# Performance work log

Hardware: AMD Instinct MI355X
Metric: run time of the kernel (lower is better)

## Reference

```python
import jax, jax.numpy as jnp
import numpy as np

T, B, E, H = 128, 1024, 1024, 1024  # batch must equal hidden (original code uses Whh @ h)


def setup_inputs() -> dict:
    key = jax.random.key(0)
    ks = jax.random.split(key, 10)
    s = 1.0 / np.sqrt(H).astype(np.float32)  # ~xavier scale, avoids gate saturation
    inp = {
        'X': jax.random.normal(ks[0], (T, B, E), dtype=jnp.float32),
        'Wii': jax.random.normal(ks[1], (E, H), dtype=jnp.float32) * s,
        'Whi': jax.random.normal(ks[2], (H, H), dtype=jnp.float32) * s,
        'bi': jnp.zeros((H,), dtype=jnp.float32),
        'Wif': jax.random.normal(ks[3], (E, H), dtype=jnp.float32) * s,
        'Whf': jax.random.normal(ks[4], (H, H), dtype=jnp.float32) * s,
        'bf': jnp.zeros((H,), dtype=jnp.float32),
        'Wig': jax.random.normal(ks[5], (E, H), dtype=jnp.float32) * s,
        'Whg': jax.random.normal(ks[6], (H, H), dtype=jnp.float32) * s,
        'bg': jnp.zeros((H,), dtype=jnp.float32),
        'Wio': jax.random.normal(ks[7], (E, H), dtype=jnp.float32) * s,
        'Who': jax.random.normal(ks[8], (H, H), dtype=jnp.float32) * s,
        'bo': jnp.zeros((H,), dtype=jnp.float32),
    }
    return inp


def reference(X, Wii, Whi, bi, Wif, Whf, bf, Wig, Whg, bg, Wio, Who, bo):
    # Faithful to the original: recurrent term is Whh @ h (NOT h @ Whh),
    # which requires batch == hidden as in the source module.
    batch = X.shape[1]
    hid = Wii.shape[1]
    h0 = jnp.zeros((batch, hid), dtype=X.dtype)
    c0 = jnp.zeros((batch, hid), dtype=X.dtype)

    def step(carry, x_t):
        h, c = carry
        i = jax.nn.sigmoid(x_t @ Wii + Whi @ h + bi)
        f = jax.nn.sigmoid(x_t @ Wif + Whf @ h + bf)
        g = jnp.tanh(x_t @ Wig + Whg @ h + bg)
        o = jax.nn.sigmoid(x_t @ Wio + Who @ h + bo)
        c_new = f * c + i * g
        h_new = o * jnp.tanh(c_new)
        return (h_new, c_new), h_new

    (h_t, c_t), hidden_sequence = jax.lax.scan(step, (h0, c0), X)
    return hidden_sequence, (h_t, c_t)
```

## Files before the change

### kernel.cpp

```cpp
#include <hip/hip_runtime.h>
#include <cstdint>

typedef __attribute__((ext_vector_type(8))) short bf16x8;
typedef __attribute__((ext_vector_type(4))) float f32x4;
typedef __attribute__((ext_vector_type(4))) unsigned int u32x4;

#define AS1 __attribute__((address_space(1)))
#define AS3 __attribute__((address_space(3)))

__device__ __forceinline__ unsigned short f2bf(float f) {
  unsigned int u = __builtin_bit_cast(unsigned int, f);
  return (unsigned short)((u + 0x7fffu + ((u >> 16) & 1u)) >> 16);
}
__device__ __forceinline__ float bf2f(unsigned short h) {
  unsigned int u = ((unsigned int)h) << 16;
  return __builtin_bit_cast(float, u);
}
__device__ __forceinline__ float sigm(float x) { return 1.f / (1.f + __expf(-x)); }
__device__ __forceinline__ float tanh_f(float x) {
  float e = __expf(2.f * x);
  return 1.f - 2.f / (e + 1.f);
}
__device__ __forceinline__ void gload16(const void* g, void* l) {
  __builtin_amdgcn_global_load_lds((const AS1 unsigned int*)g, (AS3 unsigned int*)l, 16, 0, 0);
}
__device__ __forceinline__ int swz(int e) { return e ^ (((e >> 6) & 7) << 3); }


__global__ __launch_bounds__(256) void conv_wh_kernel(
    const float4* __restrict__ w0, const float4* __restrict__ w1,
    const float4* __restrict__ w2, const float4* __restrict__ w3,
    unsigned long long* __restrict__ dst) {
  int i = blockIdx.x * 256 + threadIdx.x;
  int g = i >> 18;
  const float4* s = g == 0 ? w0 : g == 1 ? w1 : g == 2 ? w2 : w3;
  float4 v = s[i & 0x3FFFF];
  unsigned long long p = (unsigned long long)f2bf(v.x) |
                         ((unsigned long long)f2bf(v.y) << 16) |
                         ((unsigned long long)f2bf(v.z) << 32) |
                         ((unsigned long long)f2bf(v.w) << 48);
  dst[i] = p;
}

__global__ __launch_bounds__(256) void conv_wiT_kernel(
    const float* __restrict__ w0, const float* __restrict__ w1,
    const float* __restrict__ w2, const float* __restrict__ w3,
    unsigned short* __restrict__ dst) {
  __shared__ unsigned short ls[64][72];
  int bid = blockIdx.x;
  int g = bid >> 8;
  int t2 = bid & 255;
  int tj = t2 & 15, tk = t2 >> 4;
  const float* W = g == 0 ? w0 : g == 1 ? w1 : g == 2 ? w2 : w3;
  int k0 = tk * 64, j0 = tj * 64;
  int ty = threadIdx.x >> 6, tx = threadIdx.x & 63;
#pragma unroll
  for (int r = 0; r < 16; ++r) {
    int k = k0 + ty * 16 + r;
    ls[tx][ty * 16 + r] = f2bf(W[k * 1024 + j0 + tx]);
  }
  __syncthreads();
#pragma unroll
  for (int r = 0; r < 16; ++r) {
    int jl = ty * 16 + r;
    dst[(size_t)(g * 1024 + j0 + jl) * 1024 + k0 + tx] = ls[jl][tx];
  }
}

__global__ __launch_bounds__(256) void conv_bias_kernel(
    const float* __restrict__ b0, const float* __restrict__ b1,
    const float* __restrict__ b2, const float* __restrict__ b3,
    float* __restrict__ dst) {
  int i = blockIdx.x * 256 + threadIdx.x;
  const float* s = (i >> 10) == 0 ? b0 : (i >> 10) == 1 ? b1 : (i >> 10) == 2 ? b2 : b3;
  dst[i] = s[i & 1023];
}

__global__ __launch_bounds__(256) void conv_x_kernel(
    const float4* __restrict__ src, unsigned long long* __restrict__ dst, int n4) {
  int i = blockIdx.x * 256 + threadIdx.x;
  if (i < n4) {
    float4 v = src[i];
    dst[i] = (unsigned long long)f2bf(v.x) |
             ((unsigned long long)f2bf(v.y) << 16) |
             ((unsigned long long)f2bf(v.z) << 32) |
             ((unsigned long long)f2bf(v.w) << 48);
  }
}

__global__ __launch_bounds__(512) void xproj_gemm_kernel(
    const unsigned short* __restrict__ A,
    const unsigned short* __restrict__ Bt,
    unsigned short* __restrict__ C,
    int Mc) {
  __shared__ __align__(16) unsigned short smem[2][2][256 * 64];
  int xcd = blockIdx.x & 7;
  int i5 = blockIdx.x >> 3;
  int bn = xcd * 2 + (i5 & 1);
  int bm = i5 >> 1;
  int m0 = bm * 256, n0 = bn * 256;
  int tid = threadIdx.x, w = tid >> 6, lane = tid & 63;
  int wm = w >> 2, wn = w & 3;
  int l15 = lane & 15, l4 = lane >> 4;

  f32x4 acc[8][4];
#pragma unroll
  for (int i = 0; i < 8; ++i)
#pragma unroll
    for (int j = 0; j < 4; ++j) acc[i][j] = (f32x4)0.f;

  auto stageHalf = [&](int buf, int kt, int X) {
    int kk = kt * 64;
    unsigned short* dst = &smem[buf][X & 1][0];
    const unsigned short* src = (X & 1) ? Bt : A;
    int gbase = (X & 1) ? n0 : m0;
    int r0 = (X >> 1) * 128;
#pragma unroll
    for (int u = 0; u < 2; ++u) {
      int cid = u * 512 + tid;
      int rl = r0 + (cid >> 3), s = cid & 7;
      int sk = kk + ((s ^ (rl & 7)) << 3);
      gload16(&src[(size_t)(gbase + rl) * 1024 + sk],
              &dst[r0 * 64 + (u * 512 + w * 64) * 8]);
    }
  };
  auto rdA = [&](int buf, int lo, bf16x8 (&arr)[4][2]) {
#pragma unroll
    for (int mf = 0; mf < 4; ++mf)
#pragma unroll
      for (int kss = 0; kss < 2; ++kss) {
        int row = lo * 128 + wm * 64 + mf * 16 + l15;
        arr[mf][kss] =
            *(const bf16x8*)&smem[buf][0][swz(row * 64 + kss * 32 + l4 * 8)];
      }
  };
  auto rdB = [&](int buf, int lo, bf16x8 (&arr)[2][2]) {
#pragma unroll
    for (int nf = 0; nf < 2; ++nf)
#pragma unroll
      for (int kss = 0; kss < 2; ++kss) {
        int row = lo * 128 + wn * 32 + nf * 16 + l15;
        arr[nf][kss] =
            *(const bf16x8*)&smem[buf][1][swz(row * 64 + kss * 32 + l4 * 8)];
      }
  };

  bf16x8 af03[4][2], af47[4][2], bfr01[2][2], bfr23[2][2];

  auto cl1 = [&] {
#pragma unroll
    for (int mf = 0; mf < 4; ++mf)
#pragma unroll
      for (int nf = 0; nf < 2; ++nf)
#pragma unroll
        for (int k = 0; k < 2; ++k)
          acc[mf][nf] = __builtin_amdgcn_mfma_f32_16x16x32_bf16(
              af03[mf][k], bfr01[nf][k], acc[mf][nf], 0, 0, 0);
  };
  auto cl2 = [&] {
#pragma unroll
    for (int mf = 0; mf < 4; ++mf)
#pragma unroll
      for (int nf = 0; nf < 2; ++nf)
#pragma unroll
        for (int k = 0; k < 2; ++k)
          acc[4 + mf][nf] = __builtin_amdgcn_mfma_f32_16x16x32_bf16(
              af47[mf][k], bfr01[nf][k], acc[4 + mf][nf], 0, 0, 0);
  };
  auto cl3 = [&] {
#pragma unroll
    for (int mf = 0; mf < 4; ++mf)
#pragma unroll
      for (int nf = 0; nf < 2; ++nf)
#pragma unroll
        for (int k = 0; k < 2; ++k)
          acc[mf][2 + nf] = __builtin_amdgcn_mfma_f32_16x16x32_bf16(
              af03[mf][k], bfr23[nf][k], acc[mf][2 + nf], 0, 0, 0);
  };
  auto cl4 = [&] {
#pragma unroll
    for (int mf = 0; mf < 4; ++mf)
#pragma unroll
      for (int nf = 0; nf < 2; ++nf)
#pragma unroll
        for (int k = 0; k < 2; ++k)
          acc[4 + mf][2 + nf] = __builtin_amdgcn_mfma_f32_16x16x32_bf16(
              af47[mf][k], bfr23[nf][k], acc[4 + mf][2 + nf], 0, 0, 0);
  };

  stageHalf(0, 0, 0); stageHalf(0, 0, 1); stageHalf(0, 0, 2); stageHalf(0, 0, 3);

  for (int t = 0; t < 16; ++t) {
    int c = t & 1;
    asm volatile("s_waitcnt vmcnt(4)" ::: "memory");
    __builtin_amdgcn_sched_barrier(0);
    __builtin_amdgcn_s_barrier();
    __builtin_amdgcn_sched_barrier(0);
    if (t > 0) {
      __builtin_amdgcn_s_setprio(1);
      cl2();
      cl3();
      __builtin_amdgcn_s_setprio(0);
    }
    rdA(c, 0, af03);
    rdB(c, 0, bfr01);
    if (t + 1 < 16) { stageHalf(c ^ 1, t + 1, 0); stageHalf(c ^ 1, t + 1, 1); }
    if (t < 15) asm volatile("s_waitcnt vmcnt(4)" ::: "memory");
    else        asm volatile("s_waitcnt vmcnt(0)" ::: "memory");
    __builtin_amdgcn_sched_barrier(0);
    __builtin_amdgcn_s_barrier();
    __builtin_amdgcn_sched_barrier(0);
    __builtin_amdgcn_s_setprio(1);
    cl1();
    if (t > 0) cl4();
    __builtin_amdgcn_s_setprio(0);
    rdA(c, 1, af47);
    rdB(c, 1, bfr23);
    if (t + 1 < 16) { stageHalf(c ^ 1, t + 1, 2); stageHalf(c ^ 1, t + 1, 3); }
  }
  __builtin_amdgcn_s_setprio(1);
  cl2(); cl3(); cl4();
  __builtin_amdgcn_s_setprio(0);

  unsigned short* lsC = &smem[0][0][0];
#pragma unroll
  for (int h = 0; h < 2; ++h) {
    __syncthreads();
#pragma unroll
    for (int mf = 0; mf < 8; ++mf)
#pragma unroll
      for (int f = 0; f < 2; ++f) {
        int nf = h * 2 + f;
        int rowl = (mf < 4 ? wm * 64 + mf * 16 : 128 + wm * 64 + (mf - 4) * 16)
                   + l4 * 4;
        int coll = wn * 32 + f * 16 + l15;
#pragma unroll
        for (int r = 0; r < 4; ++r)
          lsC[(rowl + r) * 136 + coll] = f2bf(acc[mf][nf][r]);
      }
    __syncthreads();
#pragma unroll
    for (int u = 0; u < 8; ++u) {
      int chunk = u * 512 + tid;
      int row = chunk >> 4, c8 = chunk & 15;
      u32x4 v = *(const u32x4*)&lsC[row * 136 + c8 * 8];
      __builtin_nontemporal_store(
          v, (u32x4*)&C[(size_t)(m0 + row) * 4096 + n0 + h * 128 + c8 * 8]);
    }
  }
}

__global__ __launch_bounds__(256) void lstm_step_kernel(
    const unsigned short* __restrict__ Wh,
    const unsigned short* __restrict__ hT,
    const unsigned short* __restrict__ Xp,
    const float* __restrict__ bias,
    float* __restrict__ cst,
    float* __restrict__ out_h,
    float* __restrict__ out_ht,
    float* __restrict__ out_ct,
    unsigned short* __restrict__ hT_next,
    int isLast) {
  __shared__ unsigned short lsA[3][128 * 64];
  __shared__ unsigned short lsB[3][64 * 64];
  int bx = blockIdx.x;
  int xcd = bx & 7, idx = bx >> 3;
  int bb = xcd * 4 + (idx & 3);
  int bj = idx >> 2;
  int b0 = bb * 32, j0 = bj * 64;
  int tid = threadIdx.x, w = tid >> 6, lane = tid & 63;
  int wm = w >> 1, wn = w & 1;
  int l15 = lane & 15, l4 = lane >> 4;
  int bbase = b0 + wm * 16 + l4 * 4;

  float bias_pre[4][2];
  float c_pre[2][4];
  unsigned short xp_pre[4][2][4];
#pragma unroll
  for (int n = 0; n < 2; ++n) {
    int j = j0 + wn * 32 + n * 16 + l15;
#pragma unroll
    for (int g = 0; g < 4; ++g) bias_pre[g][n] = bias[g * 1024 + j];
#pragma unroll
    for (int r = 0; r < 4; ++r) {
      c_pre[n][r] = cst[(size_t)(bbase + r) * 1024 + j];
#pragma unroll
      for (int g = 0; g < 4; ++g)
        xp_pre[g][n][r] = Xp[(size_t)(bbase + r) * 4096 + g * 1024 + j];
    }
  }

  f32x4 acc[4][2];
#pragma unroll
  for (int g = 0; g < 4; ++g)
#pragma unroll
    for (int n = 0; n < 2; ++n) acc[g][n] = (f32x4)0.f;

  auto stage = [&](int buf, int kk) {
#pragma unroll
    for (int ld = 0; ld < 4; ++ld) {
      int cid = ld * 256 + tid;
      int r = cid >> 3, kc = (cid & 7) * 8;
      int sk = kk + (kc ^ ((r & 7) << 3));
      int grow = ((r >> 4) & 3) * 1024 + b0 + (r >> 6) * 16 + (r & 15);
      gload16(&Wh[(size_t)grow * 1024 + sk], &lsA[buf][(ld * 256 + w * 64) * 8]);
    }
#pragma unroll
    for (int u = 0; u < 2; ++u) {
      int cid = u * 256 + tid;
      int r = cid >> 3, kc = (cid & 7) * 8;
      int sk = kk + (kc ^ ((r & 7) << 3));
      gload16(&hT[(size_t)(j0 + r) * 1024 + sk], &lsB[buf][(u * 256 + w * 64) * 8]);
    }
  };
  auto compute = [&](int buf) {
    bf16x8 af[4][2], bfr[2][2];
#pragma unroll
    for (int g = 0; g < 4; ++g)
#pragma unroll
      for (int kss = 0; kss < 2; ++kss) {
        int e = (wm * 64 + g * 16 + l15) * 64 + kss * 32 + l4 * 8;
        af[g][kss] = *(const bf16x8*)&lsA[buf][swz(e)];
      }
#pragma unroll
    for (int n = 0; n < 2; ++n)
#pragma unroll
      for (int kss = 0; kss < 2; ++kss) {
        int e = (wn * 32 + n * 16 + l15) * 64 + kss * 32 + l4 * 8;
        bfr[n][kss] = *(const bf16x8*)&lsB[buf][swz(e)];
      }
    __builtin_amdgcn_s_setprio(1);
#pragma unroll
    for (int g = 0; g < 4; ++g)
#pragma unroll
      for (int n = 0; n < 2; ++n)
#pragma unroll
        for (int kss = 0; kss < 2; ++kss)
          acc[g][n] = __builtin_amdgcn_mfma_f32_16x16x32_bf16(
              af[g][kss], bfr[n][kss], acc[g][n], 0, 0, 0);
    __builtin_amdgcn_s_setprio(0);
  };

  stage(0, 0);
  stage(1, 64);
#pragma unroll
  for (int it = 0; it < 16; ++it) {
    if (it < 15) asm volatile("s_waitcnt vmcnt(6)" ::: "memory");
    else         asm volatile("s_waitcnt vmcnt(0)" ::: "memory");
    __builtin_amdgcn_sched_barrier(0);
    __builtin_amdgcn_s_barrier();
    __builtin_amdgcn_sched_barrier(0);
    if (it + 2 < 16) stage((it + 2) % 3, (it + 2) * 64);
    compute(it % 3);
    asm volatile("s_waitcnt lgkmcnt(0)" ::: "memory");
    __builtin_amdgcn_sched_barrier(0);
  }

#pragma unroll
  for (int n = 0; n < 2; ++n) {
    int j = j0 + wn * 32 + n * 16 + l15;
    float hn[4], cn[4];
#pragma unroll
    for (int r = 0; r < 4; ++r) {
      int b = bbase + r;
      float pi = acc[0][n][r] + bf2f(xp_pre[0][n][r]) + bias_pre[0][n];
      float pf = acc[1][n][r] + bf2f(xp_pre[1][n][r]) + bias_pre[1][n];
      float pg = acc[2][n][r] + bf2f(xp_pre[2][n][r]) + bias_pre[2][n];
      float po = acc[3][n][r] + bf2f(xp_pre[3][n][r]) + bias_pre[3][n];
      float ig = sigm(pi), fg = sigm(pf), gg = tanh_f(pg), og = sigm(po);
      float c_new = fg * c_pre[n][r] + ig * gg;
      cst[(size_t)b * 1024 + j] = c_new;
      cn[r] = c_new;
      hn[r] = og * tanh_f(c_new);
      __builtin_nontemporal_store(hn[r], &out_h[(size_t)b * 1024 + j]);
    }
    unsigned long long hp = (unsigned long long)f2bf(hn[0]) |
                            ((unsigned long long)f2bf(hn[1]) << 16) |
                            ((unsigned long long)f2bf(hn[2]) << 32) |
                            ((unsigned long long)f2bf(hn[3]) << 48);
    *(unsigned long long*)&hT_next[(size_t)j * 1024 + bbase] = hp;
    if (isLast) {
#pragma unroll
      for (int r = 0; r < 4; ++r) {
        int b = bbase + r;
        __builtin_nontemporal_store(hn[r], &out_ht[(size_t)b * 1024 + j]);
        __builtin_nontemporal_store(cn[r], &out_ct[(size_t)b * 1024 + j]);
      }
    }
  }
}

extern "C" void kernel_launch(void* const* d_in, const int* in_sizes, int n_in,
                              void* d_out, int out_size, void* d_ws, size_t ws_size,
                              hipStream_t stream) {
  const float* X   = (const float*)d_in[0];
  const float* Wii = (const float*)d_in[1];
  const float* Whi = (const float*)d_in[2];
  const float* bi  = (const float*)d_in[3];
  const float* Wif = (const float*)d_in[4];
  const float* Whf = (const float*)d_in[5];
  const float* bfv = (const float*)d_in[6];
  const float* Wig = (const float*)d_in[7];
  const float* Whg = (const float*)d_in[8];
  const float* bg  = (const float*)d_in[9];
  const float* Wio = (const float*)d_in[10];
  const float* Who = (const float*)d_in[11];
  const float* bo  = (const float*)d_in[12];
  float* out = (float*)d_out;

  char* wsp = (char*)d_ws;
  size_t off = 0;
  auto walloc = [&](size_t b) -> void* {
    void* p = wsp + off;
    off += (b + 255) & ~(size_t)255;
    return p;
  };
  unsigned short* WiT = (unsigned short*)walloc(4096ull * 1024 * 2);
  unsigned short* Wh  = (unsigned short*)walloc(4096ull * 1024 * 2);
  float* bias = (float*)walloc(4096 * 4);
  unsigned short* hT0 = (unsigned short*)walloc(1024ull * 1024 * 2);
  unsigned short* hT1 = (unsigned short*)walloc(1024ull * 1024 * 2);
  float* cbuf = (float*)walloc(1024ull * 1024 * 4);
  size_t fixed = off;

  long long avail = (long long)ws_size - (long long)fixed - (1ll << 20);
  int Tc = (int)(avail / (10ll << 20));
  if (Tc < 1) Tc = 1;
  if (Tc > 128) Tc = 128;
  unsigned short* Xbf = (unsigned short*)walloc((size_t)Tc * 1024 * 1024 * 2);
  unsigned short* Xp  = (unsigned short*)walloc((size_t)Tc * 1024 * 4096 * 2);

  conv_wh_kernel<<<4096, 256, 0, stream>>>((const float4*)Whi, (const float4*)Whf,
                                           (const float4*)Whg, (const float4*)Who,
                                           (unsigned long long*)Wh);
  conv_wiT_kernel<<<1024, 256, 0, stream>>>(Wii, Wif, Wig, Wio, WiT);
  conv_bias_kernel<<<16, 256, 0, stream>>>(bi, bfv, bg, bo, bias);
  hipMemsetAsync(hT0, 0, 1024ull * 1024 * 2, stream);
  hipMemsetAsync(cbuf, 0, 1024ull * 1024 * 4, stream);

  for (int t0 = 0; t0 < 128; t0 += Tc) {
    int tc = (128 - t0 < Tc) ? (128 - t0) : Tc;
    int n4 = tc * 262144;
    conv_x_kernel<<<n4 / 256, 256, 0, stream>>>(
        (const float4*)(X + (size_t)t0 * 1048576),
        (unsigned long long*)Xbf, n4);
    xproj_gemm_kernel<<<tc * 64, 512, 0, stream>>>(Xbf, WiT, Xp, tc * 1024);
    for (int i = 0; i < tc; ++i) {
      int t = t0 + i;
      lstm_step_kernel<<<512, 256, 0, stream>>>(
          Wh, (t & 1) ? hT1 : hT0,
          Xp + (size_t)i * 1024 * 4096,
          bias, cbuf,
          out + (size_t)t * 1048576,
          out + 134217728ull,
          out + 135266304ull,
          (t & 1) ? hT0 : hT1,
          (t == 127) ? 1 : 0);
    }
  }
}
```

Before: 3.702 ms.

## Restructure GEMM main loop into four-phase interleaved LDS read/MFMA pipeline

Splits each K-iteration of the bf16 MFMA GEMM into four barrier-separated phases. Each phase issues one LDS fragment read and one global-to-LDS stage, then runs one quadrant of MFMAs (cl4, cl1, cl2, cl3) on fragments loaded earlier. The goal is to spread global loads and LDS reads evenly across the loop so MFMA work overlaps memory traffic more finely. In exchange it adds more barriers and explicit lgkmcnt waits per iteration, and the vmcnt accounting is tighter, which could introduce stalls or hazards.

```diff
diff --git a/kernel.cpp b/kernel.cpp
--- a/kernel.cpp
+++ b/kernel.cpp
@@ -189,37 +189,66 @@
   };
 
   stageHalf(0, 0, 0); stageHalf(0, 0, 1); stageHalf(0, 0, 2); stageHalf(0, 0, 3);
+  asm volatile("s_waitcnt vmcnt(6)" ::: "memory");
+  __builtin_amdgcn_sched_barrier(0);
+  __builtin_amdgcn_s_barrier();
+  __builtin_amdgcn_sched_barrier(0);
 
   for (int t = 0; t < 16; ++t) {
     int c = t & 1;
-    asm volatile("s_waitcnt vmcnt(4)" ::: "memory");
+    rdA(c, 0, af03);
+    if (t + 1 < 16) stageHalf(c ^ 1, t + 1, 0);
+    if (t < 15) asm volatile("s_waitcnt vmcnt(6)" ::: "memory");
+    else        asm volatile("s_waitcnt vmcnt(4)" ::: "memory");
     __builtin_amdgcn_sched_barrier(0);
     __builtin_amdgcn_s_barrier();
+    __builtin_amdgcn_sched_barrier(0);
+    asm volatile("s_waitcnt lgkmcnt(0)" ::: "memory");
     __builtin_amdgcn_sched_barrier(0);
     if (t > 0) {
       __builtin_amdgcn_s_setprio(1);
-      cl2();
-      cl3();
+      cl4();
       __builtin_amdgcn_s_setprio(0);
     }
-    rdA(c, 0, af03);
     rdB(c, 0, bfr01);
-    if (t + 1 < 16) { stageHalf(c ^ 1, t + 1, 0); stageHalf(c ^ 1, t + 1, 1); }
-    if (t < 15) asm volatile("s_waitcnt vmcnt(4)" ::: "memory");
-    else        asm volatile("s_waitcnt vmcnt(0)" ::: "memory");
+    if (t + 1 < 16) stageHalf(c ^ 1, t + 1, 1);
+    if (t < 15) asm volatile("s_waitcnt vmcnt(6)" ::: "memory");
+    else        asm volatile("s_waitcnt vmcnt(2)" ::: "memory");
     __builtin_amdgcn_sched_barrier(0);
     __builtin_amdgcn_s_barrier();
+    __builtin_amdgcn_sched_barrier(0);
+    asm volatile("s_waitcnt lgkmcnt(0)" ::: "memory");
     __builtin_amdgcn_sched_barrier(0);
     __builtin_amdgcn_s_setprio(1);
     cl1();
-    if (t > 0) cl4();
     __builtin_amdgcn_s_setprio(0);
     rdA(c, 1, af47);
+    if (t + 1 < 16) stageHalf(c ^ 1, t + 1, 2);
+    if (t < 15) asm volatile("s_waitcnt vmcnt(6)" ::: "memory");
+    else        asm volatile("s_waitcnt vmcnt(0)" ::: "memory");
+    __builtin_amdgcn_sched_barrier(0);
+    __builtin_amdgcn_s_barrier();
+    __builtin_amdgcn_sched_barrier(0);
+    asm volatile("s_waitcnt lgkmcnt(0)" ::: "memory");
+    __builtin_amdgcn_sched_barrier(0);
+    __builtin_amdgcn_s_setprio(1);
+    cl2();
+    __builtin_amdgcn_s_setprio(0);
     rdB(c, 1, bfr23);
-    if (t + 1 < 16) { stageHalf(c ^ 1, t + 1, 2); stageHalf(c ^ 1, t + 1, 3); }
+    if (t + 1 < 16) stageHalf(c ^ 1, t + 1, 3);
+    if (t < 15) asm volatile("s_waitcnt vmcnt(6)" ::: "memory");
+    else        asm volatile("s_waitcnt vmcnt(0)" ::: "memory");
+    __builtin_amdgcn_sched_barrier(0);
+    __builtin_amdgcn_s_barrier();
+    __builtin_amdgcn_sched_barrier(0);
+    asm volatile("s_waitcnt lgkmcnt(0)" ::: "memory");
+    __builtin_amdgcn_sched_barrier(0);
+    __builtin_amdgcn_s_setprio(1);
+    cl3();
+    __builtin_amdgcn_s_setprio(0);
   }
   __builtin_amdgcn_s_setprio(1);
-  cl2(); cl3(); cl4();
+  cl4();
   __builtin_amdgcn_s_setprio(0);
 
   unsigned short* lsC = &smem[0][0][0];
```

Measured after the change: 3.366 ms. -9.1%, faster.
